# Optimization experiments

Hardware: AMD Instinct MI355X
Metric: run time of the kernel (lower is better)

Reference implementation:

```python
import jax, jax.numpy as jnp
import numpy as np

N_NODES = 50000
N_EDGES = 800000


def _gcn_conv(x, W, b, src, dst, deg_inv_sqrt, n_nodes):
    # PyG GCNConv: h = x @ W, then symmetric-normalized sum aggregation
    h = x @ W  # [N, F_out]
    norm = deg_inv_sqrt[src] * deg_inv_sqrt[dst]  # [E_aug]
    msg = h[src] * norm[:, None]  # [E_aug, F_out]
    out = jax.ops.segment_sum(msg, dst, num_segments=n_nodes)
    return out + b


def setup_inputs() -> dict:
    key = jax.random.key(0)
    k1, k2, k3, k4 = jax.random.split(key, 4)
    x = jax.random.normal(k1, (N_NODES, 128), dtype=jnp.float32)
    edge_index = jax.random.randint(k2, (2, N_EDGES), 0, N_NODES, dtype=jnp.int64)
    W1 = jax.random.normal(k3, (128, 64), dtype=jnp.float32) * (1.0 / np.sqrt(128))
    b1 = jnp.zeros((64,), dtype=jnp.float32)
    W2 = jax.random.normal(k4, (64, 32), dtype=jnp.float32) * (1.0 / np.sqrt(64))
    b2 = jnp.zeros((32,), dtype=jnp.float32)
    return {"x": x, "edge_index": edge_index, "W1": W1, "b1": b1, "W2": W2, "b2": b2}


def reference(x, edge_index, W1, b1, W2, b2):
    n_nodes = x.shape[0]
    # add self-loops (PyG GCNConv default)
    loop = jnp.arange(n_nodes, dtype=edge_index.dtype)
    src = jnp.concatenate([edge_index[0], loop])
    dst = jnp.concatenate([edge_index[1], loop])
    # symmetric normalization: deg from target index (gcn_norm)
    deg = jax.ops.segment_sum(jnp.ones_like(dst, dtype=x.dtype), dst, num_segments=n_nodes)
    deg_inv_sqrt = jnp.where(deg > 0, jax.lax.rsqrt(jnp.maximum(deg, 1.0)), 0.0)

    h = _gcn_conv(x, W1, b1, src, dst, deg_inv_sqrt, n_nodes)
    h = jax.nn.relu(h)
    # dropout is identity in eval mode (reference runs inference)
    out = _gcn_conv(h, W2, b2, src, dst, deg_inv_sqrt, n_nodes)
    return out
```

## Files before the change

kernel.cpp:

```cpp
#include <hip/hip_runtime.h>
#include <hip/hip_fp16.h>


#define F_IN 128
#define F_MID 64
#define F_OUT 32
#define NBLK 512
#define NGRP 8
#define SUBCAP 1024
#define CAP 8192
#define CAPN 64
#define EBUF 1664

#define RFL(x) __builtin_amdgcn_readfirstlane(x)

typedef int   vint4   __attribute__((ext_vector_type(4)));
typedef float vfloat4 __attribute__((ext_vector_type(4)));

__device__ __forceinline__ int ntload_i(const int* p) {
    return __builtin_nontemporal_load(p);
}
__device__ __forceinline__ uint4 ntload_u4(const uint4* p) {
    vint4 r = __builtin_nontemporal_load((const vint4*)p);
    union { vint4 v; uint4 u; } c; c.v = r; return c.u;
}
__device__ __forceinline__ float4 ntload_f4(const float4* p) {
    vfloat4 r = __builtin_nontemporal_load((const vfloat4*)p);
    union { vfloat4 v; float4 f; } c; c.v = r; return c.f;
}
__device__ __forceinline__ void ntstore_u4(uint4* p, uint4 v) {
    union { uint4 u; vint4 v; } c; c.u = v;
    __builtin_nontemporal_store(c.v, (vint4*)p);
}
__device__ __forceinline__ void ntstore_f4(float4* p, float4 v) {
    union { float4 f; vfloat4 v; } c; c.f = v;
    __builtin_nontemporal_store(c.v, (vfloat4*)p);
}

__device__ __forceinline__ void h8fma(float* a, const uint4& v, float w) {
    const __half2* hp = (const __half2*)&v;
#pragma unroll
    for (int i = 0; i < 4; ++i) {
        float2 f = __half22float2(hp[i]);
        a[2 * i]     += w * f.x;
        a[2 * i + 1] += w * f.y;
    }
}

__device__ __forceinline__ void h8unpack(float* f, const uint4& v) {
    const __half2* hp = (const __half2*)&v;
#pragma unroll
    for (int i = 0; i < 4; ++i) {
        float2 t = __half22float2(hp[i]);
        f[2 * i]     = t.x;
        f[2 * i + 1] = t.y;
    }
}

__device__ __forceinline__ uint4 pack8(const float4& a, const float4& b) {
    union { uint4 u; __half2 h[4]; } pk;
    pk.h[0] = __float22half2_rn(make_float2(a.x, a.y));
    pk.h[1] = __float22half2_rn(make_float2(a.z, a.w));
    pk.h[2] = __float22half2_rn(make_float2(b.x, b.y));
    pk.h[3] = __float22half2_rn(make_float2(b.z, b.w));
    return pk.u;
}

__global__ __launch_bounds__(256, 4) void k_build_gemm1(
    const int* __restrict__ src, const int* __restrict__ dst, int E, int chunk,
    int nbuk, int* __restrict__ cursor, int* __restrict__ esort,
    const float* __restrict__ x, const float* __restrict__ W1,
    uint4* __restrict__ g1h, int n) {
    __shared__ float xs[64 * 129];
    int t = threadIdx.x;
    if (blockIdx.x < NBLK) {
        int* cnt  = (int*)xs;
        int* off  = cnt + 256;
        int* lim  = off + 256;
        unsigned* ebuf = (unsigned*)(lim + 256);
        cnt[t] = 0;
        __syncthreads();
        int e0 = blockIdx.x * chunk;
        int e1 = min(E, e0 + chunk);
        int ne = max(0, e1 - e0);
        bool staged = (ne <= EBUF);
        if (staged) {
            for (int i = t; i < ne; i += 256) {
                int e = e0 + i;
                int s = ntload_i(src + e);
                int d = ntload_i(dst + e);
                ebuf[i] = ((unsigned)s << 16) | (unsigned)d;
                atomicAdd(&cnt[d >> 8], 1);
            }
        } else {
            for (int e = e0 + t; e < e1; e += 256)
                atomicAdd(&cnt[ntload_i(dst + e) >> 8], 1);
        }
        __syncthreads();
        int g = blockIdx.x & (NGRP - 1);
        if (t < nbuk) {
            int c = cnt[t];
            int base = t * CAP + g * SUBCAP;
            int r = c ? atomicAdd(&cursor[t * NGRP + g], c) : 0;
            off[t] = base + r;
            lim[t] = base + SUBCAP;
        }
        __syncthreads();
        if (staged) {
            for (int i = t; i < ne; i += 256) {
                unsigned p = ebuf[i];
                int d = (int)(p & 0xFFFFu);
                int bu = d >> 8;
                int pos = atomicAdd(&off[bu], 1);
                if (pos < lim[bu])
                    esort[pos] = (int)(((p >> 16) << 8) | (unsigned)(d & 255));
            }
        } else {
            for (int e = e0 + t; e < e1; e += 256) {
                int d = ntload_i(dst + e);
                int bu = d >> 8;
                int pos = atomicAdd(&off[bu], 1);
                if (pos < lim[bu])
                    esort[pos] = (ntload_i(src + e) << 8) | (d & 255);
            }
        }
        return;
    }
    int row0 = (blockIdx.x - NBLK) * 64;
    for (int i = t; i < 64 * (F_IN / 4); i += 256) {
        int r = i >> 5, k4 = i & 31;
        int gr = row0 + r;
        float4 v = make_float4(0.f, 0.f, 0.f, 0.f);
        if (gr < n) v = ntload_f4((const float4*)x + (size_t)gr * 32 + k4);
        float* p = &xs[r * 129 + k4 * 4];
        p[0] = v.x; p[1] = v.y; p[2] = v.z; p[3] = v.w;
    }
    __syncthreads();
    int w = RFL(t >> 6);
    int r = t & 63;
    const float4* W4 = (const float4*)W1;
    float4 a0 = {0.f,0.f,0.f,0.f}, a1 = a0, a2 = a0, a3 = a0;
#pragma unroll 4
    for (int k = 0; k < F_IN; ++k) {
        float xv = xs[r * 129 + k];
        float4 w0 = W4[k * 16 + w * 4 + 0];
        float4 w1 = W4[k * 16 + w * 4 + 1];
        float4 w2 = W4[k * 16 + w * 4 + 2];
        float4 w3 = W4[k * 16 + w * 4 + 3];
        a0.x += xv * w0.x; a0.y += xv * w0.y; a0.z += xv * w0.z; a0.w += xv * w0.w;
        a1.x += xv * w1.x; a1.y += xv * w1.y; a1.z += xv * w1.z; a1.w += xv * w1.w;
        a2.x += xv * w2.x; a2.y += xv * w2.y; a2.z += xv * w2.z; a2.w += xv * w2.w;
        a3.x += xv * w3.x; a3.y += xv * w3.y; a3.z += xv * w3.z; a3.w += xv * w3.w;
    }
    int gr = row0 + r;
    if (gr < n) {
        g1h[(size_t)gr * 8 + w * 2 + 0] = pack8(a0, a1);
        g1h[(size_t)gr * 8 + w * 2 + 1] = pack8(a2, a3);
    }
}

__global__ __launch_bounds__(256) void k_bucket_pad(
    const int* __restrict__ esort, const int* __restrict__ cursor, int n,
    int* __restrict__ deg, int* __restrict__ elist) {
    __shared__ int cur[256];
    int b = blockIdx.x;
    int t = threadIdx.x;
    int node0 = b << 8;
    cur[t] = 0;
    __syncthreads();
#pragma unroll
    for (int g = 0; g < NGRP; ++g) {
        int c = min(cursor[b * NGRP + g], SUBCAP);
        int s0 = b * CAP + g * SUBCAP;
        for (int e = s0 + t; e < s0 + c; e += 256) {
            int p = ntload_i(esort + e);
            int local = p & 255;
            int pos = atomicAdd(&cur[local], 1);
            if (pos < CAPN)
                elist[((node0 + local) << 6) + pos] = p >> 8;
        }
    }
    __syncthreads();
    int node = node0 + t;
    if (node < n) {
        int dg = cur[t];
        deg[node] = dg;
        int padto = dg < 32 ? 32 : min(CAPN, (dg + 7) & ~7);
        for (int p = dg; p < padto; ++p)
            elist[(node << 6) + p] = node;
    }
}

__global__ __launch_bounds__(256) void k_gather1(
    const int* __restrict__ deg, const int* __restrict__ elist,
    const uint4* __restrict__ g1h, const float* __restrict__ b1,
    uint4* __restrict__ h16, int n) {
    int wave = RFL(threadIdx.x >> 6);
    int lane = threadIdx.x & 63;
    int q    = lane & 7;
    int slot = lane >> 3;
    int d    = blockIdx.x * 4 + wave;
    if (d >= n) return;
    int base = d << 6;
    int rawdeg = deg[d];
    int s0 = ntload_i(elist + base + slot);
    int s1 = ntload_i(elist + base + 8 + slot);
    int s2 = ntload_i(elist + base + 16 + slot);
    int s3 = ntload_i(elist + base + 24 + slot);
    int dg0 = deg[s0];
    int dg1 = deg[s1];
    int dg2 = deg[s2];
    int dg3 = deg[s3];
    uint4 v0 = g1h[(size_t)s0 * 8 + q];
    uint4 v1 = g1h[(size_t)s1 * 8 + q];
    uint4 v2 = g1h[(size_t)s2 * 8 + q];
    uint4 v3 = g1h[(size_t)s3 * 8 + q];
    rawdeg = RFL(rawdeg);
    int cnt = min(rawdeg, CAPN);
    float dvd = rsqrtf((float)(rawdeg + 1));
    float a[8] = {0,0,0,0,0,0,0,0};
    float b[8] = {0,0,0,0,0,0,0,0};
    if (slot == 0) {
        uint4 v = g1h[(size_t)d * 8 + q];
        h8fma(a, v, dvd);
    }
    if (slot < cnt)      h8fma(a, v0, rsqrtf((float)(dg0 + 1)));
    if (8 + slot < cnt)  h8fma(b, v1, rsqrtf((float)(dg1 + 1)));
    if (16 + slot < cnt) h8fma(a, v2, rsqrtf((float)(dg2 + 1)));
    if (24 + slot < cnt) h8fma(b, v3, rsqrtf((float)(dg3 + 1)));
    if (cnt > 32) {
        int j = 32;
        for (; j + 8 <= cnt; j += 8) {
            int s = ntload_i(elist + base + j + slot);
            uint4 v = g1h[(size_t)s * 8 + q];
            h8fma(a, v, rsqrtf((float)(deg[s] + 1)));
        }
        if (slot < cnt - j) {
            int s = ntload_i(elist + base + j + slot);
            uint4 v = g1h[(size_t)s * 8 + q];
            h8fma(a, v, rsqrtf((float)(deg[s] + 1)));
        }
    }
#pragma unroll
    for (int i = 0; i < 8; ++i) a[i] += b[i];
#pragma unroll
    for (int i = 0; i < 8; ++i) a[i] += __shfl_xor(a[i], 8);
#pragma unroll
    for (int i = 0; i < 8; ++i) a[i] += __shfl_xor(a[i], 16);
#pragma unroll
    for (int i = 0; i < 8; ++i) a[i] += __shfl_xor(a[i], 32);
    if (slot == 0) {
        float4 bv0 = ((const float4*)b1)[q * 2 + 0];
        float4 bv1 = ((const float4*)b1)[q * 2 + 1];
        float4 o0, o1;
        o0.x = fmaxf(a[0] * dvd + bv0.x, 0.f);
        o0.y = fmaxf(a[1] * dvd + bv0.y, 0.f);
        o0.z = fmaxf(a[2] * dvd + bv0.z, 0.f);
        o0.w = fmaxf(a[3] * dvd + bv0.w, 0.f);
        o1.x = fmaxf(a[4] * dvd + bv1.x, 0.f);
        o1.y = fmaxf(a[5] * dvd + bv1.y, 0.f);
        o1.z = fmaxf(a[6] * dvd + bv1.z, 0.f);
        o1.w = fmaxf(a[7] * dvd + bv1.w, 0.f);
        ntstore_u4(h16 + (size_t)d * 8 + q, pack8(o0, o1));
    }
}

__global__ __launch_bounds__(256, 4) void k_gemm2(
    const uint4* __restrict__ h16, const float* __restrict__ W2,
    uint4* __restrict__ g2h, int n) {
    __shared__ float hs[64 * 65];
    int tid  = threadIdx.x;
    int row0 = blockIdx.x * 64;
    for (int i = tid; i < 64 * 8; i += 256) {
        int r = i >> 3, q = i & 7;
        int gr = row0 + r;
        float f[8] = {0,0,0,0,0,0,0,0};
        if (gr < n) {
            uint4 v = ntload_u4(h16 + (size_t)gr * 8 + q);
            h8unpack(f, v);
        }
        float* p = &hs[r * 65 + q * 8];
#pragma unroll
        for (int k = 0; k < 8; ++k) p[k] = f[k];
    }
    __syncthreads();
    int w = RFL(tid >> 6);
    int r = tid & 63;
    const float4* W4 = (const float4*)W2;
    float4 a0 = {0.f,0.f,0.f,0.f}, a1 = a0;
#pragma unroll 4
    for (int k = 0; k < F_MID; ++k) {
        float hv = hs[r * 65 + k];
        float4 w0 = W4[k * 8 + w * 2 + 0];
        float4 w1 = W4[k * 8 + w * 2 + 1];
        a0.x += hv * w0.x; a0.y += hv * w0.y; a0.z += hv * w0.z; a0.w += hv * w0.w;
        a1.x += hv * w1.x; a1.y += hv * w1.y; a1.z += hv * w1.z; a1.w += hv * w1.w;
    }
    int gr = row0 + r;
    if (gr < n)
        g2h[(size_t)gr * 4 + w] = pack8(a0, a1);
}

__global__ __launch_bounds__(256) void k_gather2(
    const int* __restrict__ deg, const int* __restrict__ elist,
    const uint4* __restrict__ g2h, const float* __restrict__ b2,
    float* __restrict__ out, int n) {
    int wave = RFL(threadIdx.x >> 6);
    int lane = threadIdx.x & 63;
    int q    = lane & 3;
    int slot = lane >> 2;
    int d    = blockIdx.x * 4 + wave;
    if (d >= n) return;
    int base = d << 6;
    int rawdeg = deg[d];
    int s0 = ntload_i(elist + base + slot);
    int s1 = ntload_i(elist + base + 16 + slot);
    int dg0 = deg[s0];
    int dg1 = deg[s1];
    uint4 v0 = g2h[(size_t)s0 * 4 + q];
    uint4 v1 = g2h[(size_t)s1 * 4 + q];
    rawdeg = RFL(rawdeg);
    int cnt = min(rawdeg, CAPN);
    float dvd = rsqrtf((float)(rawdeg + 1));
    float a[8] = {0,0,0,0,0,0,0,0};
    float b[8] = {0,0,0,0,0,0,0,0};
    if (slot == 0) {
        uint4 v = g2h[(size_t)d * 4 + q];
        h8fma(a, v, dvd);
    }
    if (slot < cnt)      h8fma(a, v0, rsqrtf((float)(dg0 + 1)));
    if (16 + slot < cnt) h8fma(b, v1, rsqrtf((float)(dg1 + 1)));
    if (cnt > 32) {
        int j = 32;
        for (; j + 16 <= cnt; j += 16) {
            int s = ntload_i(elist + base + j + slot);
            uint4 v = g2h[(size_t)s * 4 + q];
            h8fma(a, v, rsqrtf((float)(deg[s] + 1)));
        }
        if (slot < cnt - j) {
            int s = ntload_i(elist + base + j + slot);
            uint4 v = g2h[(size_t)s * 4 + q];
            h8fma(a, v, rsqrtf((float)(deg[s] + 1)));
        }
    }
#pragma unroll
    for (int i = 0; i < 8; ++i) a[i] += b[i];
#pragma unroll
    for (int i = 0; i < 8; ++i) a[i] += __shfl_xor(a[i], 4);
#pragma unroll
    for (int i = 0; i < 8; ++i) a[i] += __shfl_xor(a[i], 8);
#pragma unroll
    for (int i = 0; i < 8; ++i) a[i] += __shfl_xor(a[i], 16);
#pragma unroll
    for (int i = 0; i < 8; ++i) a[i] += __shfl_xor(a[i], 32);
    if (slot == 0) {
        float4 bv0 = ((const float4*)b2)[q * 2 + 0];
        float4 bv1 = ((const float4*)b2)[q * 2 + 1];
        float4 o0, o1;
        o0.x = a[0] * dvd + bv0.x;
        o0.y = a[1] * dvd + bv0.y;
        o0.z = a[2] * dvd + bv0.z;
        o0.w = a[3] * dvd + bv0.w;
        o1.x = a[4] * dvd + bv1.x;
        o1.y = a[5] * dvd + bv1.y;
        o1.z = a[6] * dvd + bv1.z;
        o1.w = a[7] * dvd + bv1.w;
        float4* O4 = (float4*)out;
        ntstore_f4(O4 + (size_t)d * 8 + q * 2 + 0, o0);
        ntstore_f4(O4 + (size_t)d * 8 + q * 2 + 1, o1);
    }
}

extern "C" void kernel_launch(void* const* d_in, const int* in_sizes, int n_in,
                              void* d_out, int out_size, void* d_ws, size_t ws_size,
                              hipStream_t stream) {
    const float* x  = (const float*)d_in[0];
    const int*   ei = (const int*)d_in[1];
    const float* W1 = (const float*)d_in[2];
    const float* b1 = (const float*)d_in[3];
    const float* W2 = (const float*)d_in[4];
    const float* b2 = (const float*)d_in[5];

    int n = in_sizes[0] / F_IN;
    int E = in_sizes[1] / 2;
    const int* src = ei;
    const int* dst = ei + E;

    int nbuk  = (n + 255) >> 8;
    int chunk = (E + NBLK - 1) / NBLK;
    int ngemm = (n + 63) / 64;

    char* ws = (char*)d_ws;
    size_t off = 0;
    auto alloc = [&](size_t bytes) {
        char* p = ws + off;
        off += (bytes + 255) & ~(size_t)255;
        return p;
    };
    int*   cursor = (int*)  alloc((size_t)nbuk * NGRP * 4);
    int*   esort  = (int*)  alloc((size_t)nbuk * CAP * 4);
    int*   deg    = (int*)  alloc((size_t)n * 4);
    int*   elist  = (int*)  alloc((size_t)n * CAPN * 4);
    uint4* g1h    = (uint4*)alloc((size_t)n * F_MID * 2);
    uint4* h16    = (uint4*)alloc((size_t)n * F_MID * 2);
    uint4* g2h    = (uint4*)alloc((size_t)n * F_OUT * 2);

    hipMemsetAsync(cursor, 0, (size_t)nbuk * NGRP * 4, stream);
    k_build_gemm1<<<NBLK + ngemm, 256, 0, stream>>>(
        src, dst, E, chunk, nbuk, cursor, esort, x, W1, g1h, n);
    k_bucket_pad<<<nbuk, 256, 0, stream>>>(esort, cursor, n, deg, elist);

    k_gather1<<<(n + 3) / 4, 256, 0, stream>>>(deg, elist, g1h, b1, h16, n);
    k_gemm2<<<(n + 63) / 64, 256, 0, stream>>>(h16, W2, g2h, n);
    k_gather2<<<(n + 3) / 4, 256, 0, stream>>>(deg, elist, g2h, b2,
                                               (float*)d_out, n);
}
```

Measured before the change: 168.8 us.

## Fuse layer-2 GEMM into layer-1 gather epilogue via wave shuffles

Removes the separate k_gemm2 kernel and the fp16 h16 intermediate buffer. Each wave now keeps its node's 64 activated features in registers after the gather reduction and multiplies them by W2 directly, broadcasting features with __shfl and reading W2 from global/cache. This avoids a write and read of the intermediate and one kernel launch. In exchange it adds per-wave GEMM work (64 shuffles plus W2 loads per node) to the gather kernel, and the launch bounds rise to 8 blocks per SM, which may limit registers.

```diff
diff --git a/kernel.cpp b/kernel.cpp
--- a/kernel.cpp
+++ b/kernel.cpp
@@ -28,10 +28,6 @@
     vfloat4 r = __builtin_nontemporal_load((const vfloat4*)p);
     union { vfloat4 v; float4 f; } c; c.v = r; return c.f;
 }
-__device__ __forceinline__ void ntstore_u4(uint4* p, uint4 v) {
-    union { uint4 u; vint4 v; } c; c.u = v;
-    __builtin_nontemporal_store(c.v, (vint4*)p);
-}
 __device__ __forceinline__ void ntstore_f4(float4* p, float4 v) {
     union { float4 f; vfloat4 v; } c; c.f = v;
     __builtin_nontemporal_store(c.v, (vfloat4*)p);
@@ -44,16 +40,6 @@
         float2 f = __half22float2(hp[i]);
         a[2 * i]     += w * f.x;
         a[2 * i + 1] += w * f.y;
-    }
-}
-
-__device__ __forceinline__ void h8unpack(float* f, const uint4& v) {
-    const __half2* hp = (const __half2*)&v;
-#pragma unroll
-    for (int i = 0; i < 4; ++i) {
-        float2 t = __half22float2(hp[i]);
-        f[2 * i]     = t.x;
-        f[2 * i + 1] = t.y;
     }
 }
 
@@ -191,10 +177,10 @@
     }
 }
 
-__global__ __launch_bounds__(256) void k_gather1(
+__global__ __launch_bounds__(256, 8) void k_gather1_gemm2(
     const int* __restrict__ deg, const int* __restrict__ elist,
     const uint4* __restrict__ g1h, const float* __restrict__ b1,
-    uint4* __restrict__ h16, int n) {
+    const float* __restrict__ W2, uint4* __restrict__ g2h, int n) {
     int wave = RFL(threadIdx.x >> 6);
     int lane = threadIdx.x & 63;
     int q    = lane & 7;
@@ -249,59 +235,38 @@
     for (int i = 0; i < 8; ++i) a[i] += __shfl_xor(a[i], 16);
 #pragma unroll
     for (int i = 0; i < 8; ++i) a[i] += __shfl_xor(a[i], 32);
-    if (slot == 0) {
+    {
         float4 bv0 = ((const float4*)b1)[q * 2 + 0];
         float4 bv1 = ((const float4*)b1)[q * 2 + 1];
-        float4 o0, o1;
-        o0.x = fmaxf(a[0] * dvd + bv0.x, 0.f);
-        o0.y = fmaxf(a[1] * dvd + bv0.y, 0.f);
-        o0.z = fmaxf(a[2] * dvd + bv0.z, 0.f);
-        o0.w = fmaxf(a[3] * dvd + bv0.w, 0.f);
-        o1.x = fmaxf(a[4] * dvd + bv1.x, 0.f);
-        o1.y = fmaxf(a[5] * dvd + bv1.y, 0.f);
-        o1.z = fmaxf(a[6] * dvd + bv1.z, 0.f);
-        o1.w = fmaxf(a[7] * dvd + bv1.w, 0.f);
-        ntstore_u4(h16 + (size_t)d * 8 + q, pack8(o0, o1));
-    }
-}
-
-__global__ __launch_bounds__(256, 4) void k_gemm2(
-    const uint4* __restrict__ h16, const float* __restrict__ W2,
-    uint4* __restrict__ g2h, int n) {
-    __shared__ float hs[64 * 65];
-    int tid  = threadIdx.x;
-    int row0 = blockIdx.x * 64;
-    for (int i = tid; i < 64 * 8; i += 256) {
-        int r = i >> 3, q = i & 7;
-        int gr = row0 + r;
-        float f[8] = {0,0,0,0,0,0,0,0};
-        if (gr < n) {
-            uint4 v = ntload_u4(h16 + (size_t)gr * 8 + q);
-            h8unpack(f, v);
-        }
-        float* p = &hs[r * 65 + q * 8];
-#pragma unroll
-        for (int k = 0; k < 8; ++k) p[k] = f[k];
-    }
-    __syncthreads();
-    int w = RFL(tid >> 6);
-    int r = tid & 63;
-    const float4* W4 = (const float4*)W2;
-    float4 a0 = {0.f,0.f,0.f,0.f}, a1 = a0;
-#pragma unroll 4
-    for (int k = 0; k < F_MID; ++k) {
-        float hv = hs[r * 65 + k];
-        float4 w0 = W4[k * 8 + w * 2 + 0];
-        float4 w1 = W4[k * 8 + w * 2 + 1];
-        a0.x += hv * w0.x; a0.y += hv * w0.y; a0.z += hv * w0.z; a0.w += hv * w0.w;
-        a1.x += hv * w1.x; a1.y += hv * w1.y; a1.z += hv * w1.z; a1.w += hv * w1.w;
-    }
-    int gr = row0 + r;
-    if (gr < n)
-        g2h[(size_t)gr * 4 + w] = pack8(a0, a1);
-}
-
-__global__ __launch_bounds__(256) void k_gather2(
+        a[0] = fmaxf(a[0] * dvd + bv0.x, 0.f);
+        a[1] = fmaxf(a[1] * dvd + bv0.y, 0.f);
+        a[2] = fmaxf(a[2] * dvd + bv0.z, 0.f);
+        a[3] = fmaxf(a[3] * dvd + bv0.w, 0.f);
+        a[4] = fmaxf(a[4] * dvd + bv1.x, 0.f);
+        a[5] = fmaxf(a[5] * dvd + bv1.y, 0.f);
+        a[6] = fmaxf(a[6] * dvd + bv1.z, 0.f);
+        a[7] = fmaxf(a[7] * dvd + bv1.w, 0.f);
+    }
+    float o0 = 0.f, o1 = 0.f, o2 = 0.f, o3 = 0.f;
+    const float4* W24 = (const float4*)W2;
+    for (int qq = 0; qq < 8; ++qq) {
+#pragma unroll
+        for (int i = 0; i < 8; ++i) {
+            float hh = __shfl(a[i], qq);
+            float4 wv = W24[(8 * qq + i) * 8 + slot];
+            o0 += hh * wv.x; o1 += hh * wv.y;
+            o2 += hh * wv.z; o3 += hh * wv.w;
+        }
+    }
+    if (q == 0) {
+        union { uint2 u; __half2 h[2]; } pk;
+        pk.h[0] = __float22half2_rn(make_float2(o0, o1));
+        pk.h[1] = __float22half2_rn(make_float2(o2, o3));
+        ((uint2*)g2h)[(size_t)d * 8 + slot] = pk.u;
+    }
+}
+
+__global__ __launch_bounds__(256, 8) void k_gather2(
     const int* __restrict__ deg, const int* __restrict__ elist,
     const uint4* __restrict__ g2h, const float* __restrict__ b2,
     float* __restrict__ out, int n) {
@@ -402,7 +367,6 @@
     int*   deg    = (int*)  alloc((size_t)n * 4);
     int*   elist  = (int*)  alloc((size_t)n * CAPN * 4);
     uint4* g1h    = (uint4*)alloc((size_t)n * F_MID * 2);
-    uint4* h16    = (uint4*)alloc((size_t)n * F_MID * 2);
     uint4* g2h    = (uint4*)alloc((size_t)n * F_OUT * 2);
 
     hipMemsetAsync(cursor, 0, (size_t)nbuk * NGRP * 4, stream);
@@ -410,8 +374,8 @@
         src, dst, E, chunk, nbuk, cursor, esort, x, W1, g1h, n);
     k_bucket_pad<<<nbuk, 256, 0, stream>>>(esort, cursor, n, deg, elist);
 
-    k_gather1<<<(n + 3) / 4, 256, 0, stream>>>(deg, elist, g1h, b1, h16, n);
-    k_gemm2<<<(n + 63) / 64, 256, 0, stream>>>(h16, W2, g2h, n);
+    k_gather1_gemm2<<<(n + 3) / 4, 256, 0, stream>>>(
+        deg, elist, g1h, b1, W2, g2h, n);
     k_gather2<<<(n + 3) / 4, 256, 0, stream>>>(deg, elist, g2h, b2,
                                                (float*)d_out, n);
 }
```

Measured after the change: 244.0 us. 44.5% more time.
